# Performance work log

Hardware: AMD Instinct MI355X
Metric: run time of the kernel (lower is better)

## Reference

```python
import jax, jax.numpy as jnp
import numpy as np

SEQ_LEN = 4096      # config.seq_len (num_blocks=1 so PosPerBlock == seq_len)
EMB = 3             # config.filter_emb_dim
FILTER_ORDER = 16   # config.filter_order
CH = 768            # HeadSizeOrderMinus1 = hidden_dim/num_heads*(order-1)
BATCH = 16
SHIFT = 0.0
MODULATE = True
USE_BIAS = True
FAST_DECAY_PCT = 0.3
SLOW_DECAY_PCT = 1.5
TARGET = 0.01


def _pos_emb(L):
    # PositionalEmbedding: t in [0,1], complex exponential bands
    t = jnp.linspace(0.0, 1.0, L)                      # [L]
    bands = (EMB - 1) // 2                              # = 1
    t_rescaled = jnp.linspace(0.0, float(L - 1), L)     # [L]
    w = 2.0 * jnp.pi * t_rescaled / L                   # [L]
    f = jnp.linspace(1e-4, float(max(bands - 1, 0)), bands)  # [bands]
    z_c = jnp.exp(-1j * f[None, :] * w[:, None])        # [L, bands]
    z = jnp.concatenate([t[:, None], jnp.real(z_c), jnp.imag(z_c)], axis=-1)  # [L, EMB]
    return z.astype(jnp.float32), t.astype(jnp.float32)


def _implicit_filter(L, w1, b1, w2, b2, w3, b3, freq, deltas_abs):
    z, t = _pos_emb(L)
    # MLP with trainable Sin activation (freq shared across layers)
    h = jnp.sin(freq * (z @ w1.T + b1))                 # [L, FILTER_ORDER]
    h = jnp.sin(freq * (h @ w2.T + b2))                 # [L, FILTER_ORDER]
    h = h @ w3.T + b3                                   # [L, CH]
    if MODULATE:
        decay = jnp.exp(-t[:, None] * deltas_abs[None, :])  # [L, CH]
        h = h * (decay + SHIFT)
    return h


def fft_conv(u, k):
    seqlen = u.shape[-2]
    fft_size = 2 * seqlen
    u_f = jnp.fft.rfft(u.astype(jnp.float32), n=fft_size, axis=-2)
    k_f = jnp.fft.rfft(k.astype(jnp.float32), n=fft_size, axis=-2) / fft_size
    y = jnp.fft.irfft(u_f * k_f, n=fft_size, axis=-2)[..., :seqlen, :]
    return y.astype(u.dtype)


def setup_inputs() -> dict:
    key = jax.random.key(0)
    ks = jax.random.split(key, 8)
    u = jax.random.normal(ks[0], (BATCH, SEQ_LEN, CH), dtype=jnp.float32)
    w1 = jax.random.normal(ks[1], (FILTER_ORDER, EMB), dtype=jnp.float32) * 0.5
    b1 = jax.random.normal(ks[2], (FILTER_ORDER,), dtype=jnp.float32) * 0.1
    w2 = jax.random.normal(ks[3], (FILTER_ORDER, FILTER_ORDER), dtype=jnp.float32) * 0.25
    b2 = jax.random.normal(ks[4], (FILTER_ORDER,), dtype=jnp.float32) * 0.1
    w3 = jax.random.normal(ks[5], (CH, FILTER_ORDER), dtype=jnp.float32) * 0.25
    b3 = jax.random.normal(ks[6], (CH,), dtype=jnp.float32) * 0.1
    freq = jnp.ones((FILTER_ORDER,), dtype=jnp.float32)  # Sin.init with w=1
    # ExponentialModulation.init
    max_decay = np.log(TARGET) / FAST_DECAY_PCT
    min_decay = np.log(TARGET) / SLOW_DECAY_PCT
    deltas_abs = jnp.abs(jnp.linspace(min_decay, max_decay, CH)).astype(jnp.float32)
    bias = jax.random.normal(ks[7], (CH,), dtype=jnp.float32)
    return {"u": u, "w1": w1, "b1": b1, "w2": w2, "b2": b2,
            "w3": w3, "b3": b3, "freq": freq, "deltas_abs": deltas_abs, "bias": bias}


def reference(u, w1, b1, w2, b2, w3, b3, freq, deltas_abs, bias):
    L = u.shape[-2]
    k = _implicit_filter(L, w1, b1, w2, b2, w3, b3, freq, deltas_abs)  # [L, CH]
    y = fft_conv(u, k)
    if USE_BIAS:
        y = y + u * bias  # bias broadcast over [B, L, CH]
    return y
```

## Files before the change

kernel.cpp:

```cpp
#include <hip/hip_runtime.h>
#include <hip/hip_bf16.h>

#define SEQ   4096
#define NFFT  8192
#define NCH   768
#define NB    16
#define KGST  4104
#define LDSN  4368

typedef float cf __attribute__((ext_vector_type(2)));
typedef float f4 __attribute__((ext_vector_type(4)));

__device__ __forceinline__ int phys(int p) { return p + (p >> 4) + (p >> 8); }
__device__ __forceinline__ int br12(int k) { return (int)(__brev((unsigned)k) >> 20); }

constexpr int stepFor(int G) { return G == 256 ? 273 : (G == 16 ? 17 : 1); }

constexpr int BR4[16] = {0,8,4,12,2,10,6,14,1,9,5,13,3,11,7,15};

__device__ __forceinline__ cf cmul_wi(cf a, cf w, cf iw) {
  cf axx = __builtin_shufflevector(a, a, 0, 0);
  cf ayy = __builtin_shufflevector(a, a, 1, 1);
  return axx * w + ayy * iw;
}
__device__ __forceinline__ cf icmul(cf a) { return cf{-a.y, a.x}; }
__device__ __forceinline__ cf cmul(cf a, cf b) { return cmul_wi(a, b, icmul(b)); }
__device__ __forceinline__ cf cmul_cj(cf a, cf z) {
  return cmul_wi(a, cf{z.x, -z.y}, cf{z.y, z.x});
}

#define CMULC(a, WX, WY) cmul_wi(a, cf{(WX),(WY)}, cf{-(WY),(WX)})

#define C1X 0.9238795325112867f
#define C1Y (-0.3826834323650898f)
#define C2X 0.7071067811865476f
#define C2Y (-0.7071067811865476f)
#define C3X 0.3826834323650898f
#define C3Y (-0.9238795325112867f)

#define BF_F(a, b, WX, WY) { cf t_ = a - b; a = a + b; b = CMULC(t_, WX, WY); }
#define BF_F1(a, b)        { cf t_ = a - b; a = a + b; b = t_; }
#define BF_FJ(a, b)        { cf t_ = a - b; a = a + b; b = cf{t_.y, -t_.x}; }
#define BF_I(a, b, WX, WY) { cf t_ = cmul_wi(b, cf{(WX),-(WY)}, cf{(WY),(WX)}); b = a - t_; a = a + t_; }
#define BF_I1(a, b)        { cf t_ = b; b = a - t_; a = a + t_; }
#define BF_IJ(a, b)        { cf t_ = cf{-b.y, b.x}; b = a - t_; a = a + t_; }

__device__ __forceinline__ void dft16_f_tail(cf v[16]) {
  BF_F1(v[0], v[4]);            BF_F(v[1], v[5],  C2X, C2Y);
  BF_FJ(v[2], v[6]);            BF_F(v[3], v[7], -C2X, C2Y);
  BF_F1(v[8], v[12]);           BF_F(v[9], v[13], C2X, C2Y);
  BF_FJ(v[10], v[14]);          BF_F(v[11], v[15], -C2X, C2Y);
  BF_F1(v[0], v[2]);  BF_FJ(v[1], v[3]);
  BF_F1(v[4], v[6]);  BF_FJ(v[5], v[7]);
  BF_F1(v[8], v[10]); BF_FJ(v[9], v[11]);
  BF_F1(v[12], v[14]); BF_FJ(v[13], v[15]);
  BF_F1(v[0], v[1]);  BF_F1(v[2], v[3]);
  BF_F1(v[4], v[5]);  BF_F1(v[6], v[7]);
  BF_F1(v[8], v[9]);  BF_F1(v[10], v[11]);
  BF_F1(v[12], v[13]); BF_F1(v[14], v[15]);
}

__device__ __forceinline__ void dft16_f(cf v[16]) {
  BF_F1(v[0], v[8]);
  BF_F(v[1], v[9],  C1X, C1Y);
  BF_F(v[2], v[10], C2X, C2Y);
  BF_F(v[3], v[11], C3X, C3Y);
  BF_FJ(v[4], v[12]);
  BF_F(v[5], v[13], -C3X, C3Y);
  BF_F(v[6], v[14], -C2X, C2Y);
  BF_F(v[7], v[15], -C1X, C1Y);
  dft16_f_tail(v);
}

__device__ __forceinline__ void dft16_i(cf v[16]) {
  BF_I1(v[0], v[1]);  BF_I1(v[2], v[3]);
  BF_I1(v[4], v[5]);  BF_I1(v[6], v[7]);
  BF_I1(v[8], v[9]);  BF_I1(v[10], v[11]);
  BF_I1(v[12], v[13]); BF_I1(v[14], v[15]);
  BF_I1(v[0], v[2]);  BF_IJ(v[1], v[3]);
  BF_I1(v[4], v[6]);  BF_IJ(v[5], v[7]);
  BF_I1(v[8], v[10]); BF_IJ(v[9], v[11]);
  BF_I1(v[12], v[14]); BF_IJ(v[13], v[15]);
  BF_I1(v[0], v[4]);            BF_I(v[1], v[5],  C2X, C2Y);
  BF_IJ(v[2], v[6]);            BF_I(v[3], v[7], -C2X, C2Y);
  BF_I1(v[8], v[12]);           BF_I(v[9], v[13], C2X, C2Y);
  BF_IJ(v[10], v[14]);          BF_I(v[11], v[15], -C2X, C2Y);
  BF_I1(v[0], v[8]);
  BF_I(v[1], v[9],  C1X, C1Y);
  BF_I(v[2], v[10], C2X, C2Y);
  BF_I(v[3], v[11], C3X, C3Y);
  BF_IJ(v[4], v[12]);
  BF_I(v[5], v[13], -C3X, C3Y);
  BF_I(v[6], v[14], -C2X, C2Y);
  BF_I(v[7], v[15], -C1X, C1Y);
}

__device__ __forceinline__ void twiddle_apply(cf v[16], cf w1) {
  cf iw1 = icmul(w1);
  cf w2 = cmul_wi(w1, w1, iw1),  iw2 = icmul(w2);
  cf w4 = cmul_wi(w2, w2, iw2),  iw4 = icmul(w4);
  cf w8 = cmul_wi(w4, w4, iw4),  iw8 = icmul(w8);
  cf w3 = cmul_wi(w1, w2, iw2);
  cf w5 = cmul_wi(w1, w4, iw4);
  cf w6 = cmul_wi(w2, w4, iw4);
  cf w7 = cmul_wi(w3, w4, iw4);
  cf w9  = cmul_wi(w1, w8, iw8);
  cf w10 = cmul_wi(w2, w8, iw8);
  cf w11 = cmul_wi(w3, w8, iw8);
  cf w12 = cmul_wi(w4, w8, iw8);
  cf w13 = cmul_wi(w5, w8, iw8);
  cf w14 = cmul_wi(w6, w8, iw8);
  cf w15 = cmul_wi(w7, w8, iw8);
  v[BR4[1]]  = cmul_wi(v[BR4[1]],  w1,  iw1);
  v[BR4[2]]  = cmul_wi(v[BR4[2]],  w2,  iw2);
  v[BR4[3]]  = cmul(v[BR4[3]],  w3);
  v[BR4[4]]  = cmul_wi(v[BR4[4]],  w4,  iw4);
  v[BR4[5]]  = cmul(v[BR4[5]],  w5);
  v[BR4[6]]  = cmul(v[BR4[6]],  w6);
  v[BR4[7]]  = cmul(v[BR4[7]],  w7);
  v[BR4[8]]  = cmul_wi(v[BR4[8]],  w8,  iw8);
  v[BR4[9]]  = cmul(v[BR4[9]],  w9);
  v[BR4[10]] = cmul(v[BR4[10]], w10);
  v[BR4[11]] = cmul(v[BR4[11]], w11);
  v[BR4[12]] = cmul(v[BR4[12]], w12);
  v[BR4[13]] = cmul(v[BR4[13]], w13);
  v[BR4[14]] = cmul(v[BR4[14]], w14);
  v[BR4[15]] = cmul(v[BR4[15]], w15);
}

__device__ __forceinline__ void twiddle_f(cf v[16], int i, float invNP) {
  float sn, cs; __sincosf(-6.283185307179586f * (float)i * invNP, &sn, &cs);
  twiddle_apply(v, cf{cs, sn});
}
__device__ __forceinline__ void twiddle_i(cf v[16], int i, float invNP) {
  float sn, cs; __sincosf(6.283185307179586f * (float)i * invNP, &sn, &cs);
  twiddle_apply(v, cf{cs, sn});
}

__device__ __forceinline__ void pass_f_first(cf* X, int tid) {
  cf* Xp = X + phys(tid);
  cf v[16];
  #pragma unroll
  for (int m = 0; m < 8; ++m) v[m] = Xp[273 * m];
  v[8]  = v[0];
  v[9]  = CMULC(v[1],  C1X, C1Y);
  v[10] = CMULC(v[2],  C2X, C2Y);
  v[11] = CMULC(v[3],  C3X, C3Y);
  v[12] = cf{v[4].y, -v[4].x};
  v[13] = CMULC(v[5], -C3X, C3Y);
  v[14] = CMULC(v[6], -C2X, C2Y);
  v[15] = CMULC(v[7], -C1X, C1Y);
  dft16_f_tail(v);
  if (tid) twiddle_f(v, tid, 1.0f / 4096.0f);
  #pragma unroll
  for (int s = 0; s < 16; ++s) Xp[273 * s] = v[s];
}

template<int NP>
__device__ __forceinline__ void pass_f(cf* X, int tid) {
  constexpr int G = NP / 16;
  constexpr int ST = stepFor(G);
  int i = tid & (G - 1);
  int base = (tid & ~(G - 1)) * 16 + i;
  cf* Xp = X + phys(base);
  cf v[16];
  #pragma unroll
  for (int m = 0; m < 16; ++m) v[m] = Xp[ST * m];
  dft16_f(v);
  if (G > 1 && i) twiddle_f(v, i, 1.0f / (float)NP);
  #pragma unroll
  for (int s = 0; s < 16; ++s) Xp[ST * s] = v[s];
}

template<int NP>
__device__ __forceinline__ void pass_i(cf* X, int tid) {
  constexpr int G = NP / 16;
  constexpr int ST = stepFor(G);
  int i = tid & (G - 1);
  int base = (tid & ~(G - 1)) * 16 + i;
  cf* Xp = X + phys(base);
  cf v[16];
  #pragma unroll
  for (int s = 0; s < 16; ++s) v[s] = Xp[ST * s];
  if (G > 1 && i) twiddle_i(v, i, 1.0f / (float)NP);
  dft16_i(v);
  #pragma unroll
  for (int m = 0; m < 16; ++m) Xp[ST * m] = v[m];
}

__device__ __forceinline__ void fft_forward(cf* X, int tid) {
  pass_f_first(X, tid); __syncthreads();
  pass_f<256>(X, tid);  __syncthreads();
  pass_f<16>(X, tid);   __syncthreads();
}
__device__ __forceinline__ void fft_inverse(cf* X, int tid) {
  pass_i<16>(X, tid);   __syncthreads();
  pass_i<256>(X, tid);  __syncthreads();
  pass_i<4096>(X, tid);
}

__device__ __forceinline__ void unpack_pair(cf Zk, cf Zq, float c_, float s_,
                                            cf& Xk, cf& Xm) {
  float Ex = 0.5f*(Zk.x + Zq.x), Ey = 0.5f*(Zk.y - Zq.y);
  float Ox = 0.5f*(Zk.y + Zq.y), Oy = 0.5f*(Zq.x - Zk.x);
  Xk = cf{Ex + c_*Ox + s_*Oy,  Ey + c_*Oy - s_*Ox};
  Xm = cf{Ex - c_*Ox - s_*Oy, -Ey + c_*Oy - s_*Ox};
}

__device__ __forceinline__ cf bf16pair_to_cf(unsigned int v) {
  return cf{__uint_as_float(v << 16), __uint_as_float(v & 0xFFFF0000u)};
}
__device__ __forceinline__ unsigned int cf_to_bf16pair(cf z) {
  unsigned int a = __float_as_uint(z.x), b = __float_as_uint(z.y);
  a = (a + 0x7FFFu + ((a >> 16) & 1u)) >> 16;
  b = (b + 0x7FFFu + ((b >> 16) & 1u)) & 0xFFFF0000u;
  return a | b;
}
__device__ __forceinline__ unsigned int pack_bf16(float x, float y) {
  return cf_to_bf16pair(cf{x, y});
}

__device__ __forceinline__ float mlp_eval(int n, const float* sw1, const float* sb1,
    const float* sw2, const float* sb2, const float* sfq, const float* sw3,
    float B3, float D) {
  float t = (float)n * (1.0f / 4095.0f);
  float fw = 1e-4f * 6.283185307179586f * (float)n / 4096.0f;
  float sfw, cfw; __sincosf(fw, &sfw, &cfw);
  float z0 = t, z1 = cfw, z2 = -sfw;
  float h1[16], h2[16];
  #pragma unroll
  for (int r = 0; r < 16; ++r)
    h1[r] = __sinf(sfq[r] * (z0 * sw1[3*r] + z1 * sw1[3*r+1] + z2 * sw1[3*r+2] + sb1[r]));
  #pragma unroll
  for (int r = 0; r < 16; ++r) {
    float acc = sb2[r];
    #pragma unroll
    for (int s = 0; s < 16; ++s) acc += h1[s] * sw2[16*r + s];
    h2[r] = __sinf(sfq[r] * acc);
  }
  float k = B3;
  #pragma unroll
  for (int r = 0; r < 16; ++r) k += h2[r] * sw3[r];
  return k * __expf(-t * D);
}

__global__ __launch_bounds__(256) void filter_fft_kernel(
    const float* __restrict__ w1, const float* __restrict__ b1,
    const float* __restrict__ w2, const float* __restrict__ b2,
    const float* __restrict__ w3, const float* __restrict__ b3,
    const float* __restrict__ freq, const float* __restrict__ deltas,
    uint2* __restrict__ Kg) {
  __shared__ cf X[LDSN];
  __shared__ float sw1[48], sb1[16], sw2[256], sb2[16], sfq[16], sw3[16];
  int tid = threadIdx.x;
  int c = blockIdx.x;
  if (tid < 48) sw1[tid] = w1[tid];
  if (tid < 16) { sb1[tid] = b1[tid]; sb2[tid] = b2[tid]; sfq[tid] = freq[tid];
                  sw3[tid] = w3[(size_t)c * 16 + tid]; }
  sw2[tid] = w2[tid];
  float B3 = b3[c], D = deltas[c];
  __syncthreads();

  {
    cf* Xp = X + phys(tid);
    #pragma unroll
    for (int j = 0; j < 8; ++j) {
      int n2 = tid + 256 * j;
      float k0 = mlp_eval(2*n2,     sw1, sb1, sw2, sb2, sfq, sw3, B3, D);
      float k1 = mlp_eval(2*n2 + 1, sw1, sb1, sw2, sb2, sfq, sw3, B3, D);
      Xp[273 * j] = cf{k0, k1};
    }
  }

  fft_forward(X, tid);

  const float SC = 1.0f / 33554432.0f;
  uint2* Kc = Kg + (size_t)c * KGST;
  for (int k = tid; k <= 2048; k += 256) {
    int q = (4096 - k) & 4095;
    cf Zk = X[phys(br12(k))], Zq = X[phys(br12(q))];
    float s_, c_; __sincosf((float)k * (3.14159265358979e0f / 4096.0f), &s_, &c_);
    cf Xk, Xm;
    unpack_pair(Zk, Zq, c_, s_, Xk, Xm);
    float f0 = SC * 0.5f * (1.0f - s_);
    float f1 = SC * 0.5f * (1.0f + s_);
    float f2 = SC * 0.5f * c_;
    cf Xmc = cf{Xm.x, -Xm.y};
    cf Xkc = cf{Xk.x, -Xk.y};
    cf G1k = f0 * Xk + f1 * Xmc;
    cf G2k = f2 * icmul(Xk - Xmc);
    cf G1q = f0 * Xm + f1 * Xkc;
    cf G2q = -f2 * icmul(Xm - Xkc);
    Kc[k] = uint2{cf_to_bf16pair(G1k), cf_to_bf16pair(G2k)};
    Kc[q] = uint2{cf_to_bf16pair(G1q), cf_to_bf16pair(G2q)};
  }
}

__global__ __launch_bounds__(256) void transpose_in(
    const float* __restrict__ u, __hip_bfloat16* __restrict__ ut) {
  __shared__ float tile[64][65];
  int i0 = blockIdx.x * 64, c0 = blockIdx.y * 64, b = blockIdx.z;
  int tx = threadIdx.x & 15, ty = threadIdx.x >> 4;
  const float* up = u + ((size_t)b * SEQ + i0) * NCH + c0;
  #pragma unroll
  for (int rr = 0; rr < 4; ++rr) {
    int row = ty + 16 * rr;
    f4 v = *(const f4*)&up[(size_t)row * NCH + tx * 4];
    tile[tx*4 + 0][row] = v.x;
    tile[tx*4 + 1][row] = v.y;
    tile[tx*4 + 2][row] = v.z;
    tile[tx*4 + 3][row] = v.w;
  }
  __syncthreads();
  __hip_bfloat16* op = ut + ((size_t)b * NCH + c0) * SEQ + i0;
  #pragma unroll
  for (int cp = 0; cp < 4; ++cp) {
    int c = ty + 16 * cp;
    uint2 o;
    o.x = pack_bf16(tile[c][tx*4 + 0], tile[c][tx*4 + 1]);
    o.y = pack_bf16(tile[c][tx*4 + 2], tile[c][tx*4 + 3]);
    *(uint2*)&op[(size_t)c * SEQ + tx * 4] = o;
  }
}

__global__ __launch_bounds__(256) void conv_kernel(
    __hip_bfloat16* __restrict__ ut, const uint2* __restrict__ Kg) {
  __shared__ cf X[LDSN];
  int tid = threadIdx.x;
  int wg  = blockIdx.x;
  int id  = (wg & 7) * (NCH * NB / 8) + (wg >> 3);
  int c   = id >> 4;
  int b   = id & 15;
  unsigned int* row = (unsigned int*)(ut + ((size_t)b * NCH + c) * SEQ);
  const uint2* Kc = Kg + (size_t)c * KGST;

  {
    cf* Xp = X + phys(tid);
    #pragma unroll
    for (int j = 0; j < 8; ++j) Xp[273 * j] = bf16pair_to_cf(row[tid + 256 * j]);
  }

  fft_forward(X, tid);

  for (int k = tid; k <= 2048; k += 256) {
    int q  = (4096 - k) & 4095;
    int p  = phys(br12(k));
    int pq = phys(br12(q));
    cf Zk = X[p], Zq = X[pq];
    uint2 gk = Kc[k];
    uint2 gq = Kc[q];
    cf G1k = bf16pair_to_cf(gk.x), G2k = bf16pair_to_cf(gk.y);
    cf G1q = bf16pair_to_cf(gq.x), G2q = bf16pair_to_cf(gq.y);
    X[p]  = cmul(G1k, Zk) + cmul_cj(G2k, Zq);
    X[pq] = cmul(G1q, Zq) + cmul_cj(G2q, Zk);
  }
  __syncthreads();

  fft_inverse(X, tid);

  {
    cf* Xp = X + phys(tid);
    #pragma unroll
    for (int j = 0; j < 8; ++j) row[tid + 256 * j] = cf_to_bf16pair(Xp[273 * j]);
  }
}

__global__ __launch_bounds__(256) void transpose_out(
    const __hip_bfloat16* __restrict__ yt, const float* __restrict__ u,
    const float* __restrict__ bias, float* __restrict__ y) {
  __shared__ float tile[64][65];
  int i0 = blockIdx.x * 64, c0 = blockIdx.y * 64, b = blockIdx.z;
  int tx = threadIdx.x & 15, ty = threadIdx.x >> 4;
  const __hip_bfloat16* ypb = yt + ((size_t)b * NCH + c0) * SEQ + i0;
  #pragma unroll
  for (int cp = 0; cp < 4; ++cp) {
    int c = ty + 16 * cp;
    uint2 v = *(const uint2*)&ypb[(size_t)c * SEQ + tx * 4];
    cf lo = bf16pair_to_cf(v.x), hi = bf16pair_to_cf(v.y);
    tile[tx*4 + 0][c] = lo.x;
    tile[tx*4 + 1][c] = lo.y;
    tile[tx*4 + 2][c] = hi.x;
    tile[tx*4 + 3][c] = hi.y;
  }
  __syncthreads();
  f4 bi = *(const f4*)&bias[c0 + tx * 4];
  const float* up = u + ((size_t)b * SEQ + i0) * NCH + c0;
  float* op = y + ((size_t)b * SEQ + i0) * NCH + c0;
  #pragma unroll
  for (int rp = 0; rp < 4; ++rp) {
    int row = ty + 16 * rp;
    f4 uv = __builtin_nontemporal_load((const f4*)&up[(size_t)row * NCH + tx * 4]);
    f4 o;
    o.x = tile[row][tx*4 + 0] + uv.x * bi.x;
    o.y = tile[row][tx*4 + 1] + uv.y * bi.y;
    o.z = tile[row][tx*4 + 2] + uv.z * bi.z;
    o.w = tile[row][tx*4 + 3] + uv.w * bi.w;
    __builtin_nontemporal_store(o, (f4*)&op[(size_t)row * NCH + tx * 4]);
  }
}

extern "C" void kernel_launch(void* const* d_in, const int* in_sizes, int n_in,
                              void* d_out, int out_size, void* d_ws, size_t ws_size,
                              hipStream_t stream) {
  const float* u      = (const float*)d_in[0];
  const float* w1     = (const float*)d_in[1];
  const float* b1     = (const float*)d_in[2];
  const float* w2     = (const float*)d_in[3];
  const float* b2     = (const float*)d_in[4];
  const float* w3     = (const float*)d_in[5];
  const float* b3     = (const float*)d_in[6];
  const float* freq   = (const float*)d_in[7];
  const float* deltas = (const float*)d_in[8];
  const float* bias   = (const float*)d_in[9];
  float* out = (float*)d_out;

  const size_t utB = (size_t)NB * NCH * SEQ * 2;
  __hip_bfloat16* ut = (__hip_bfloat16*)d_ws;
  uint2* Kg = (uint2*)((char*)d_ws + utB);

  filter_fft_kernel<<<dim3(NCH), dim3(256), 0, stream>>>(w1, b1, w2, b2, w3, b3, freq, deltas, Kg);
  transpose_in<<<dim3(SEQ / 64, NCH / 64, NB), dim3(256), 0, stream>>>(u, ut);
  conv_kernel<<<dim3(NCH * NB), dim3(256), 0, stream>>>(ut, Kg);
  transpose_out<<<dim3(SEQ / 64, NCH / 64, NB), dim3(256), 0, stream>>>(ut, u, bias, out);
}
```

Baseline: 441.2 us.

## Fuse transposes into conv kernel, processing four channels per workgroup from registers

Removes the separate transpose_in and transpose_out kernels and the bf16 intermediate buffer. Each workgroup reads four adjacent channels of u straight from the [B,L,C] layout as float4 strided loads and runs the FFT convolution for each channel in turn. It adds the bias term and writes the float4 results directly. This cuts global memory round trips and bf16 rounding of the input, but the strided 16-byte accesses have poor coalescing, the 64 live floats per thread raise register pressure, and there are 4x fewer workgroups.

```diff
diff --git a/kernel.cpp b/kernel.cpp
--- a/kernel.cpp
+++ b/kernel.cpp
@@ -216,9 +216,6 @@
   b = (b + 0x7FFFu + ((b >> 16) & 1u)) & 0xFFFF0000u;
   return a | b;
 }
-__device__ __forceinline__ unsigned int pack_bf16(float x, float y) {
-  return cf_to_bf16pair(cf{x, y});
-}
 
 __device__ __forceinline__ float mlp_eval(int n, const float* sw1, const float* sb1,
     const float* sw2, const float* sb2, const float* sfq, const float* sw3,
@@ -296,106 +293,73 @@
   }
 }
 
-__global__ __launch_bounds__(256) void transpose_in(
-    const float* __restrict__ u, __hip_bfloat16* __restrict__ ut) {
-  __shared__ float tile[64][65];
-  int i0 = blockIdx.x * 64, c0 = blockIdx.y * 64, b = blockIdx.z;
-  int tx = threadIdx.x & 15, ty = threadIdx.x >> 4;
-  const float* up = u + ((size_t)b * SEQ + i0) * NCH + c0;
-  #pragma unroll
-  for (int rr = 0; rr < 4; ++rr) {
-    int row = ty + 16 * rr;
-    f4 v = *(const f4*)&up[(size_t)row * NCH + tx * 4];
-    tile[tx*4 + 0][row] = v.x;
-    tile[tx*4 + 1][row] = v.y;
-    tile[tx*4 + 2][row] = v.z;
-    tile[tx*4 + 3][row] = v.w;
-  }
-  __syncthreads();
-  __hip_bfloat16* op = ut + ((size_t)b * NCH + c0) * SEQ + i0;
-  #pragma unroll
-  for (int cp = 0; cp < 4; ++cp) {
-    int c = ty + 16 * cp;
-    uint2 o;
-    o.x = pack_bf16(tile[c][tx*4 + 0], tile[c][tx*4 + 1]);
-    o.y = pack_bf16(tile[c][tx*4 + 2], tile[c][tx*4 + 3]);
-    *(uint2*)&op[(size_t)c * SEQ + tx * 4] = o;
-  }
-}
-
-__global__ __launch_bounds__(256) void conv_kernel(
-    __hip_bfloat16* __restrict__ ut, const uint2* __restrict__ Kg) {
+__global__ __launch_bounds__(256) void fused_conv4(
+    const float* __restrict__ u, const uint2* __restrict__ Kg,
+    const float* __restrict__ bias, float* __restrict__ y) {
   __shared__ cf X[LDSN];
   int tid = threadIdx.x;
   int wg  = blockIdx.x;
-  int id  = (wg & 7) * (NCH * NB / 8) + (wg >> 3);
-  int c   = id >> 4;
+  int id  = (wg & 7) * (NCH / 4 * NB / 8) + (wg >> 3);
+  int cg  = id >> 4;
   int b   = id & 15;
-  unsigned int* row = (unsigned int*)(ut + ((size_t)b * NCH + c) * SEQ);
-  const uint2* Kc = Kg + (size_t)c * KGST;
-
-  {
-    cf* Xp = X + phys(tid);
-    #pragma unroll
-    for (int j = 0; j < 8; ++j) Xp[273 * j] = bf16pair_to_cf(row[tid + 256 * j]);
-  }
-
-  fft_forward(X, tid);
-
-  for (int k = tid; k <= 2048; k += 256) {
-    int q  = (4096 - k) & 4095;
-    int p  = phys(br12(k));
-    int pq = phys(br12(q));
-    cf Zk = X[p], Zq = X[pq];
-    uint2 gk = Kc[k];
-    uint2 gq = Kc[q];
-    cf G1k = bf16pair_to_cf(gk.x), G2k = bf16pair_to_cf(gk.y);
-    cf G1q = bf16pair_to_cf(gq.x), G2q = bf16pair_to_cf(gq.y);
-    X[p]  = cmul(G1k, Zk) + cmul_cj(G2k, Zq);
-    X[pq] = cmul(G1q, Zq) + cmul_cj(G2q, Zk);
-  }
-  __syncthreads();
-
-  fft_inverse(X, tid);
-
-  {
-    cf* Xp = X + phys(tid);
-    #pragma unroll
-    for (int j = 0; j < 8; ++j) row[tid + 256 * j] = cf_to_bf16pair(Xp[273 * j]);
-  }
-}
-
-__global__ __launch_bounds__(256) void transpose_out(
-    const __hip_bfloat16* __restrict__ yt, const float* __restrict__ u,
-    const float* __restrict__ bias, float* __restrict__ y) {
-  __shared__ float tile[64][65];
-  int i0 = blockIdx.x * 64, c0 = blockIdx.y * 64, b = blockIdx.z;
-  int tx = threadIdx.x & 15, ty = threadIdx.x >> 4;
-  const __hip_bfloat16* ypb = yt + ((size_t)b * NCH + c0) * SEQ + i0;
-  #pragma unroll
-  for (int cp = 0; cp < 4; ++cp) {
-    int c = ty + 16 * cp;
-    uint2 v = *(const uint2*)&ypb[(size_t)c * SEQ + tx * 4];
-    cf lo = bf16pair_to_cf(v.x), hi = bf16pair_to_cf(v.y);
-    tile[tx*4 + 0][c] = lo.x;
-    tile[tx*4 + 1][c] = lo.y;
-    tile[tx*4 + 2][c] = hi.x;
-    tile[tx*4 + 3][c] = hi.y;
-  }
-  __syncthreads();
-  f4 bi = *(const f4*)&bias[c0 + tx * 4];
-  const float* up = u + ((size_t)b * SEQ + i0) * NCH + c0;
-  float* op = y + ((size_t)b * SEQ + i0) * NCH + c0;
-  #pragma unroll
-  for (int rp = 0; rp < 4; ++rp) {
-    int row = ty + 16 * rp;
-    f4 uv = __builtin_nontemporal_load((const f4*)&up[(size_t)row * NCH + tx * 4]);
-    f4 o;
-    o.x = tile[row][tx*4 + 0] + uv.x * bi.x;
-    o.y = tile[row][tx*4 + 1] + uv.y * bi.y;
-    o.z = tile[row][tx*4 + 2] + uv.z * bi.z;
-    o.w = tile[row][tx*4 + 3] + uv.w * bi.w;
-    __builtin_nontemporal_store(o, (f4*)&op[(size_t)row * NCH + tx * 4]);
+  int c0  = cg * 4;
+
+  const float* ub = u + (size_t)b * SEQ * NCH + c0;
+  float*       yb = y + (size_t)b * SEQ * NCH + c0;
+  f4 bi4 = *(const f4*)&bias[c0];
+
+  f4 ue[8], uo[8];
+  #pragma unroll
+  for (int j = 0; j < 8; ++j) {
+    int l = 2 * tid + 512 * j;
+    ue[j] = *(const f4*)&ub[(size_t)l * NCH];
+    uo[j] = *(const f4*)&ub[(size_t)(l + 1) * NCH];
+  }
+
+  #pragma unroll
+  for (int ch = 0; ch < 4; ++ch) {
+    {
+      cf* Xp = X + phys(tid);
+      #pragma unroll
+      for (int j = 0; j < 8; ++j) Xp[273 * j] = cf{ue[j][ch], uo[j][ch]};
+    }
+
+    fft_forward(X, tid);
+
+    const uint2* Kc = Kg + (size_t)(c0 + ch) * KGST;
+    for (int k = tid; k <= 2048; k += 256) {
+      int q  = (4096 - k) & 4095;
+      int p  = phys(br12(k));
+      int pq = phys(br12(q));
+      cf Zk = X[p], Zq = X[pq];
+      uint2 gk = Kc[k];
+      uint2 gq = Kc[q];
+      cf G1k = bf16pair_to_cf(gk.x), G2k = bf16pair_to_cf(gk.y);
+      cf G1q = bf16pair_to_cf(gq.x), G2q = bf16pair_to_cf(gq.y);
+      X[p]  = cmul(G1k, Zk) + cmul_cj(G2k, Zq);
+      X[pq] = cmul(G1q, Zq) + cmul_cj(G2q, Zk);
+    }
+    __syncthreads();
+
+    fft_inverse(X, tid);
+
+    {
+      cf* Xp = X + phys(tid);
+      float bi = bi4[ch];
+      #pragma unroll
+      for (int j = 0; j < 8; ++j) {
+        cf z = Xp[273 * j];
+        ue[j][ch] = z.x + ue[j][ch] * bi;
+        uo[j][ch] = z.y + uo[j][ch] * bi;
+      }
+    }
+  }
+
+  #pragma unroll
+  for (int j = 0; j < 8; ++j) {
+    int l = 2 * tid + 512 * j;
+    *(f4*)&yb[(size_t)l * NCH]       = ue[j];
+    *(f4*)&yb[(size_t)(l + 1) * NCH] = uo[j];
   }
 }
 
@@ -414,12 +378,8 @@
   const float* bias   = (const float*)d_in[9];
   float* out = (float*)d_out;
 
-  const size_t utB = (size_t)NB * NCH * SEQ * 2;
-  __hip_bfloat16* ut = (__hip_bfloat16*)d_ws;
-  uint2* Kg = (uint2*)((char*)d_ws + utB);
+  uint2* Kg = (uint2*)d_ws;
 
   filter_fft_kernel<<<dim3(NCH), dim3(256), 0, stream>>>(w1, b1, w2, b2, w3, b3, freq, deltas, Kg);
-  transpose_in<<<dim3(SEQ / 64, NCH / 64, NB), dim3(256), 0, stream>>>(u, ut);
-  conv_kernel<<<dim3(NCH * NB), dim3(256), 0, stream>>>(ut, Kg);
-  transpose_out<<<dim3(SEQ / 64, NCH / 64, NB), dim3(256), 0, stream>>>(ut, u, bias, out);
-}
+  fused_conv4<<<dim3(NCH / 4 * NB), dim3(256), 0, stream>>>(u, Kg, bias, out);
+}
```

New measurement: 844.2 us. +91.4%, slower.
